# Performance work log

Measured on AMD Instinct MI355X. Metric: run time of the kernel, lower is better.

## Reference

```python
import jax, jax.numpy as jnp
import numpy as np

B, T, E = 64, 64, 256
S, ENC = 128, 1024
RNN, ATT, DENSE = 1024, 1024, 8000


def setup_inputs() -> dict:
    key = jax.random.key(0)
    ks = jax.random.split(key, 16)
    s = 0.02
    return {
        "initial_input": jax.random.normal(ks[0], (B, T, E), jnp.float32),
        "hidden": jax.random.normal(ks[1], (B, RNN), jnp.float32),
        "cell": jax.random.normal(ks[2], (B, RNN), jnp.float32),
        "encoder_output": jax.random.normal(ks[3], (B, S, ENC), jnp.float32),
        "W1": jax.random.normal(ks[4], (RNN, ATT), jnp.float32) * s,
        "b1": jnp.zeros((ATT,), jnp.float32),
        "W2": jax.random.normal(ks[5], (ENC, ATT), jnp.float32) * s,
        "b2": jnp.zeros((ATT,), jnp.float32),
        "V": jax.random.normal(ks[6], (ATT, 1), jnp.float32) * s,
        "bV": jnp.zeros((1,), jnp.float32),
        "kernel": jax.random.normal(ks[7], (ENC + E, 4 * RNN), jnp.float32) * s,
        "rkernel": jax.random.normal(ks[8], (RNN, 4 * RNN), jnp.float32) * s,
        "bias": jnp.zeros((4 * RNN,), jnp.float32),
        "Wd": jax.random.normal(ks[9], (RNN, DENSE), jnp.float32) * s,
        "bd": jnp.zeros((DENSE,), jnp.float32),
        "seq_len": T,
    }


def _decode(initial_input, hidden, cell, encoder_output,
            W1, b1, W2, b2, V, bV, kernel, rkernel, bias, Wd, bd):
    # Keys W2(encoder_output) are step-independent: precompute once. [B,S,ATT]
    keys = jnp.einsum('bse,ea->bsa', encoder_output, W2) + b2

    def step(carry, x_t):
        h, c = carry
        # Bahdanau attention: score = V^T tanh(W1 h + W2 enc)
        q = h @ W1 + b1                                  # [B,ATT]
        score = jnp.tanh(q[:, None, :] + keys) @ V + bV   # [B,S,1]
        attn = jax.nn.softmax(score, axis=1)              # [B,S,1]
        ctx = jnp.sum(attn * encoder_output, axis=1)      # [B,ENC]
        # LSTM cell (Keras gate order i,f,g,o; sigmoid/tanh activations)
        inp = jnp.concatenate([ctx, x_t], axis=-1)        # [B,ENC+E]
        z = inp @ kernel + h @ rkernel + bias              # [B,4*RNN]
        i, f, g, o = jnp.split(z, 4, axis=-1)
        i = jax.nn.sigmoid(i)
        f = jax.nn.sigmoid(f)
        g = jnp.tanh(g)
        o = jax.nn.sigmoid(o)
        c_new = f * c + i * g
        h_new = o * jnp.tanh(c_new)
        logits = h_new @ Wd + bd                           # [B,DENSE]
        return (h_new, c_new), logits

    xs = jnp.swapaxes(initial_input, 0, 1)  # [T,B,E]
    (h, c), logits = jax.lax.scan(step, (hidden, cell), xs)
    outputs = jnp.swapaxes(logits, 0, 1)    # [B,T,DENSE]
    return outputs, h, c


def reference(initial_input, hidden, cell, encoder_output,
              W1, b1, W2, b2, V, bV, kernel, rkernel, bias, Wd, bd, seq_len):
    # seq_len == initial_input.shape[1] (static); the Python loop in the
    # original is expressed as an efficient lax.scan over decode steps.
    return _decode(initial_input[:, :seq_len, :], hidden, cell, encoder_output,
                   W1, b1, W2, b2, V, bV, kernel, rkernel, bias, Wd, bd)
```

## Files before the change

kernel.cpp:

```cpp
#include <hip/hip_runtime.h>
#include <hip/hip_bf16.h>
#include <stdint.h>


typedef __attribute__((ext_vector_type(8))) short short8;
typedef __attribute__((ext_vector_type(4))) float floatx4;
typedef __attribute__((ext_vector_type(4))) unsigned short ushortx4;

__device__ __forceinline__ float b2f(unsigned short u) {
    union { unsigned int i; float f; } v; v.i = ((unsigned int)u) << 16; return v.f;
}
__device__ __forceinline__ unsigned short f2b(float f) {
    union { float f; unsigned int i; } v; v.f = f;
    unsigned int r = v.i + 0x7fffu + ((v.i >> 16) & 1u);
    return (unsigned short)(r >> 16);
}
__device__ __forceinline__ float ftanh(float x) {
    x = fminf(15.f, fmaxf(-15.f, x));
    float e = __expf(2.f * x);
    return (e - 1.f) * __builtin_amdgcn_rcpf(e + 1.f);
}
__device__ __forceinline__ float vtanh(float x) {
    return __builtin_fmaf(-2.f, __builtin_amdgcn_rcpf(__expf(2.f * x) + 1.f), 1.f);
}
__device__ __forceinline__ float fsig(float x) {
    return __builtin_amdgcn_rcpf(1.f + __expf(-x));
}
__device__ __forceinline__ void ld_lds16(const void* g, void* l) {
    __builtin_amdgcn_global_load_lds((const __attribute__((address_space(1))) void*)g,
                                     (__attribute__((address_space(3))) void*)l, 16, 0, 0);
}

__device__ __forceinline__ void tr_tile(
    float (*tile)[33], const float* __restrict__ src, int srcld,
    unsigned short* __restrict__ dst, int dstld, int coloff, int perm,
    int bx, int by, int tid)
{
    const int k0 = by * 32, n0 = bx * 32;
    const int r = tid >> 3, c = (tid & 7) * 4;
    int n = n0 + c;
    int cn = perm ? ((((n >> 4) & 3) << 10) | ((n >> 6) << 4) | (n & 15)) : n;
    float4 v = *(const float4*)&src[(size_t)(k0 + r) * srcld + cn];
    tile[r][c + 0] = v.x; tile[r][c + 1] = v.y;
    tile[r][c + 2] = v.z; tile[r][c + 3] = v.w;
    __syncthreads();
    const int nr = tid >> 3, kc = (tid & 7) * 4;
    ushortx4 o;
    o[0] = f2b(tile[kc + 0][nr]);
    o[1] = f2b(tile[kc + 1][nr]);
    o[2] = f2b(tile[kc + 2][nr]);
    o[3] = f2b(tile[kc + 3][nr]);
    *(ushortx4*)&dst[(size_t)(n0 + nr) * dstld + coloff + k0 + kc] = o;
}

__global__ __launch_bounds__(256) void prep_all(
    const float* __restrict__ W2, unsigned short* __restrict__ W2T,
    const float* __restrict__ W1, unsigned short* __restrict__ W1T,
    const float* __restrict__ Wk, const float* __restrict__ rk,
    unsigned short* __restrict__ KRT,
    const float* __restrict__ Wd, unsigned short* __restrict__ WdT,
    const float* __restrict__ enc, unsigned short* __restrict__ enc_bf,
    const float* __restrict__ hidden, const float* __restrict__ cell,
    const float* __restrict__ x,
    float* __restrict__ cb, unsigned short* __restrict__ hbf,
    unsigned short* __restrict__ Axc0)
{
    __shared__ float tile[32][33];
    const int lid = blockIdx.x, tid = threadIdx.x;
    if (lid < 1024) {
        tr_tile(tile, W2, 1024, W2T, 1024, 0, 0, lid & 31, lid >> 5, tid);
    } else if (lid < 2048) {
        int l = lid - 1024;
        tr_tile(tile, W1, 1024, W1T, 1024, 0, 0, l & 31, l >> 5, tid);
    } else if (lid < 6144) {
        int l = lid - 2048;
        tr_tile(tile, Wk, 4096, KRT, 2304, 0, 1, l & 127, l >> 7, tid);
    } else if (lid < 7168) {
        int l = lid - 6144;
        tr_tile(tile, Wk + 1024 * 4096, 4096, KRT, 2304, 1024, 1, l & 127, l >> 7, tid);
    } else if (lid < 11264) {
        int l = lid - 7168;
        tr_tile(tile, rk, 4096, KRT, 2304, 1280, 1, l & 127, l >> 7, tid);
    } else if (lid < 19264) {
        int l = lid - 11264;
        tr_tile(tile, Wd, 8000, WdT, 1024, 0, 0, l % 250, l / 250, tid);
    } else if (lid < 27456) {
        int i = (lid - 19264) * 256 + tid;
        float4 v = ((const float4*)enc)[i];
        ushortx4 o;
        o[0] = f2b(v.x); o[1] = f2b(v.y); o[2] = f2b(v.z); o[3] = f2b(v.w);
        ((ushortx4*)enc_bf)[i] = o;
    } else if (lid < 27712) {
        int idx = (lid - 27456) * 256 + tid;
        float h = hidden[idx], c = cell[idx];
        cb[idx] = c;
        unsigned short hb = f2b(h);
        hbf[idx] = hb;
        Axc0[(idx >> 10) * 2304 + 1280 + (idx & 1023)] = hb;
    } else {
        int p = (lid - 27712) * 256 + tid;
        int b = p >> 7, e2 = (p & 127) * 2;
        float x0 = x[((size_t)b * 64) * 256 + e2];
        float x1 = x[((size_t)b * 64) * 256 + e2 + 1];
        *(unsigned int*)&Axc0[b * 2304 + 1024 + e2] =
            (unsigned int)f2b(x0) | ((unsigned int)f2b(x1) << 16);
    }
}

__global__ __launch_bounds__(256) void gemm_bf16_128(
    const unsigned short* __restrict__ A, int lda,
    const unsigned short* __restrict__ BT, int ldbt, int K,
    float* __restrict__ Cf, unsigned short* __restrict__ Cb,
    int ldc, int ncols, const float* __restrict__ bias, int swz)
{
    __shared__ __align__(16) unsigned short As[128 * 32];
    __shared__ __align__(16) unsigned short Bs[128 * 32];
    const int tid = threadIdx.x, wave = tid >> 6, lane = tid & 63;
    const int q = lane >> 4, lm = lane & 15;
    const int wr = wave >> 1, wc = wave & 1;
    int bx = blockIdx.x, by = blockIdx.y;
    if (swz == 1) {
        int bid = by * gridDim.x + bx;
        int xcd = bid & 7, l = bid >> 3;
        bx = xcd * 8 + (l & 7);
        by = l >> 3;
    } else if (swz == 2) {
        int bid = by * gridDim.x + bx;
        int xcd = bid & 7, m = bid >> 3;
        by = xcd * 8 + (m & 7);
        bx = m >> 3;
    }
    const int m0 = by * 128, n0 = bx * 128;
    const int srow = lane >> 2;
    const int gch = (lane & 3) ^ ((lane >> 3) & 3);
    const unsigned short* Ag0 = A + (size_t)(m0 + wave * 32 + srow) * lda + gch * 8;
    const unsigned short* Ag1 = Ag0 + (size_t)16 * lda;
    const unsigned short* Bg0 = BT + (size_t)(n0 + wave * 32 + srow) * ldbt + gch * 8;
    const unsigned short* Bg1 = Bg0 + (size_t)16 * ldbt;
    unsigned short* Al0 = &As[(wave * 32) * 32];
    unsigned short* Al1 = &As[(wave * 32 + 16) * 32];
    unsigned short* Bl0 = &Bs[(wave * 32) * 32];
    unsigned short* Bl1 = &Bs[(wave * 32 + 16) * 32];

    const floatx4 z4 = {0.f, 0.f, 0.f, 0.f};
    floatx4 acc[4][4];
#pragma unroll
    for (int i = 0; i < 4; i++)
#pragma unroll
        for (int j = 0; j < 4; j++) acc[i][j] = z4;
    const int ach = ((q ^ ((lm >> 1) & 3))) * 8;

    for (int kb = 0; kb < K; kb += 32) {
        ld_lds16(Ag0 + kb, Al0);
        ld_lds16(Ag1 + kb, Al1);
        ld_lds16(Bg0 + kb, Bl0);
        ld_lds16(Bg1 + kb, Bl1);
        __syncthreads();
        short8 a[4], b[4];
#pragma unroll
        for (int i = 0; i < 4; i++) a[i] = *(const short8*)&As[(wr * 64 + i * 16 + lm) * 32 + ach];
#pragma unroll
        for (int j = 0; j < 4; j++) b[j] = *(const short8*)&Bs[(wc * 64 + j * 16 + lm) * 32 + ach];
#pragma unroll
        for (int i = 0; i < 4; i++)
#pragma unroll
            for (int j = 0; j < 4; j++)
                acc[i][j] = __builtin_amdgcn_mfma_f32_16x16x32_bf16(a[i], b[j], acc[i][j], 0, 0, 0);
        __syncthreads();
    }
    const int rb = m0 + wr * 64 + q * 4;
#pragma unroll
    for (int i = 0; i < 4; i++) {
#pragma unroll
        for (int j = 0; j < 4; j++) {
            int col = n0 + wc * 64 + j * 16 + lm;
            if (col < ncols) {
                float bv = bias ? bias[col] : 0.f;
#pragma unroll
                for (int r = 0; r < 4; r++) {
                    float v = acc[i][j][r] + bv;
                    size_t idx = (size_t)(rb + i * 16 + r) * ldc + col;
                    if (Cf) Cf[idx] = v;
                    if (Cb) Cb[idx] = f2b(v);
                }
            }
        }
    }
}

__global__ __launch_bounds__(256) void gemm64_split(
    const unsigned short* __restrict__ A, int lda,
    const unsigned short* __restrict__ BT, int ldbt,
    int kchunk, float* __restrict__ Cpart, int ldc)
{
    __shared__ __align__(16) unsigned short As[4][64 * 32];
    __shared__ __align__(16) unsigned short Bs[4][64 * 32];
    const int tid = threadIdx.x, wave = tid >> 6, lane = tid & 63;
    const int q = lane >> 4, lm = lane & 15;
    const int n0 = blockIdx.x * 64;
    const int k0 = blockIdx.z * kchunk;
    const int srow = lane >> 2;
    const int gch = (lane & 3) ^ ((lane >> 3) & 3);
    const unsigned short* Ag = A + (size_t)(wave * 16 + srow) * lda + k0 + gch * 8;
    const unsigned short* Bg = BT + (size_t)(n0 + wave * 16 + srow) * ldbt + k0 + gch * 8;
    const int loff = (wave * 16) * 32;
    const floatx4 z4 = {0.f, 0.f, 0.f, 0.f};
    floatx4 acc0 = z4, acc1 = z4, acc2 = z4, acc3 = z4;
    const int ach = ((q ^ ((lm >> 1) & 3))) * 8;
    const int nit = kchunk >> 5;

#pragma unroll
    for (int p = 0; p < 3; ++p) {
        if (p < nit) {
            ld_lds16(Ag + p * 32, &As[p][loff]);
            ld_lds16(Bg + p * 32, &Bs[p][loff]);
        }
    }
    for (int it = 0; it < nit; ++it) {
        const int st = it & 3;
        if (it + 2 < nit)      asm volatile("s_waitcnt vmcnt(4)\n\ts_barrier" ::: "memory");
        else if (it + 1 < nit) asm volatile("s_waitcnt vmcnt(2)\n\ts_barrier" ::: "memory");
        else                   asm volatile("s_waitcnt vmcnt(0)\n\ts_barrier" ::: "memory");
        if (it + 3 < nit) {
            const int sn = (it + 3) & 3;
            ld_lds16(Ag + (it + 3) * 32, &As[sn][loff]);
            ld_lds16(Bg + (it + 3) * 32, &Bs[sn][loff]);
        }
        short8 a  = *(const short8*)&As[st][(wave * 16 + lm) * 32 + ach];
        short8 b0 = *(const short8*)&Bs[st][(0 * 16 + lm) * 32 + ach];
        short8 b1 = *(const short8*)&Bs[st][(1 * 16 + lm) * 32 + ach];
        short8 b2 = *(const short8*)&Bs[st][(2 * 16 + lm) * 32 + ach];
        short8 b3 = *(const short8*)&Bs[st][(3 * 16 + lm) * 32 + ach];
        acc0 = __builtin_amdgcn_mfma_f32_16x16x32_bf16(a, b0, acc0, 0, 0, 0);
        acc1 = __builtin_amdgcn_mfma_f32_16x16x32_bf16(a, b1, acc1, 0, 0, 0);
        acc2 = __builtin_amdgcn_mfma_f32_16x16x32_bf16(a, b2, acc2, 0, 0, 0);
        acc3 = __builtin_amdgcn_mfma_f32_16x16x32_bf16(a, b3, acc3, 0, 0, 0);
    }
    float* Cp = Cpart + (size_t)blockIdx.z * 64 * ldc;
    const int rb = wave * 16 + q * 4;
    floatx4 accs[4] = {acc0, acc1, acc2, acc3};
#pragma unroll
    for (int i = 0; i < 4; i++) {
        int col = n0 + i * 16 + lm;
#pragma unroll
        for (int r = 0; r < 4; r++) Cp[(size_t)(rb + r) * ldc + col] = accs[i][r];
    }
}

__global__ __launch_bounds__(256) void attn_scores(
    const float* __restrict__ qp, const float* __restrict__ b1,
    const unsigned short* __restrict__ keys,
    const float* __restrict__ V, const float* __restrict__ bV,
    float* __restrict__ sc)
{
    __shared__ float qs[1024];
    __shared__ float vs[1024];
    const int b = blockIdx.y, sg = blockIdx.x;
    const int tid = threadIdx.x, wave = tid >> 6, lane = tid & 63;
    {
        float4 a0 = ((const float4*)(qp + (size_t)b * 1024))[tid];
        float4 a1 = ((const float4*)(qp + 65536 + (size_t)b * 1024))[tid];
        float4 a2 = ((const float4*)(qp + 131072 + (size_t)b * 1024))[tid];
        float4 a3 = ((const float4*)(qp + 196608 + (size_t)b * 1024))[tid];
        float4 ab = ((const float4*)b1)[tid];
        float4 av = ((const float4*)V)[tid];
        float4 r;
        r.x = a0.x + a1.x + a2.x + a3.x + ab.x;
        r.y = a0.y + a1.y + a2.y + a3.y + ab.y;
        r.z = a0.z + a1.z + a2.z + a3.z + ab.z;
        r.w = a0.w + a1.w + a2.w + a3.w + ab.w;
        *(float4*)&qs[tid * 4] = r;
        *(float4*)&vs[tid * 4] = av;
    }
    __syncthreads();
    float qr[16], vr[16];
#pragma unroll
    for (int i = 0; i < 4; i++) {
        float4 tq = *(const float4*)&qs[lane * 16 + i * 4];
        float4 tv = *(const float4*)&vs[lane * 16 + i * 4];
        qr[i * 4 + 0] = tq.x; qr[i * 4 + 1] = tq.y; qr[i * 4 + 2] = tq.z; qr[i * 4 + 3] = tq.w;
        vr[i * 4 + 0] = tv.x; vr[i * 4 + 1] = tv.y; vr[i * 4 + 2] = tv.z; vr[i * 4 + 3] = tv.w;
    }
    const float bv0 = bV[0];
#pragma unroll
    for (int i = 0; i < 4; i++) {
        const int s = sg * 16 + wave * 4 + i;
        const uint4* kp = (const uint4*)(keys + ((size_t)(b * 128 + s)) * 1024 + lane * 16);
        uint4 k0 = kp[0], k1 = kp[1];
        float kf[16];
        kf[0] = b2f((unsigned short)(k0.x & 0xffff)); kf[1] = b2f((unsigned short)(k0.x >> 16));
        kf[2] = b2f((unsigned short)(k0.y & 0xffff)); kf[3] = b2f((unsigned short)(k0.y >> 16));
        kf[4] = b2f((unsigned short)(k0.z & 0xffff)); kf[5] = b2f((unsigned short)(k0.z >> 16));
        kf[6] = b2f((unsigned short)(k0.w & 0xffff)); kf[7] = b2f((unsigned short)(k0.w >> 16));
        kf[8] = b2f((unsigned short)(k1.x & 0xffff)); kf[9] = b2f((unsigned short)(k1.x >> 16));
        kf[10] = b2f((unsigned short)(k1.y & 0xffff)); kf[11] = b2f((unsigned short)(k1.y >> 16));
        kf[12] = b2f((unsigned short)(k1.z & 0xffff)); kf[13] = b2f((unsigned short)(k1.z >> 16));
        kf[14] = b2f((unsigned short)(k1.w & 0xffff)); kf[15] = b2f((unsigned short)(k1.w >> 16));
        float part = 0.f;
#pragma unroll
        for (int j = 0; j < 16; j++) part += vr[j] * vtanh(qr[j] + kf[j]);
#pragma unroll
        for (int off = 32; off; off >>= 1) part += __shfl_xor(part, off);
        if (lane == 0) sc[b * 128 + s] = part + bv0;
    }
}

__global__ __launch_bounds__(256) void softmax_ctx(
    const float* __restrict__ sc, const unsigned short* __restrict__ enc_bf,
    unsigned short* __restrict__ Axc_t)
{
    __shared__ float attnv[128];
    __shared__ float red[4][64][2];
    __shared__ float ssum_s;
    const int b = blockIdx.y, chunk = blockIdx.x;
    const int tid = threadIdx.x, wave = tid >> 6, lane = tid & 63;
    if (tid < 128) attnv[tid] = __expf(sc[b * 128 + tid]);
    __syncthreads();
    if (tid < 64) {
        float s2 = attnv[tid] + attnv[tid + 64];
#pragma unroll
        for (int off = 32; off; off >>= 1) s2 += __shfl_xor(s2, off);
        if (tid == 0) ssum_s = s2;
    }
    const unsigned int* ep = (const unsigned int*)enc_bf + (size_t)b * 65536 + chunk * 64 + lane;
    __syncthreads();
    float ax = 0.f, ay = 0.f;
#pragma unroll 8
    for (int i = 0; i < 32; i++) {
        int s = wave * 32 + i;
        float a = attnv[s];
        unsigned int u = ep[(size_t)s * 512];
        ax += a * b2f((unsigned short)(u & 0xffff));
        ay += a * b2f((unsigned short)(u >> 16));
    }
    red[wave][lane][0] = ax; red[wave][lane][1] = ay;
    __syncthreads();
    if (tid < 64) {
        float rs = __builtin_amdgcn_rcpf(ssum_s);
        float fx = (red[0][lane][0] + red[1][lane][0] + red[2][lane][0] + red[3][lane][0]) * rs;
        float fy = (red[0][lane][1] + red[1][lane][1] + red[2][lane][1] + red[3][lane][1]) * rs;
        *(unsigned int*)&Axc_t[b * 2304 + chunk * 128 + lane * 2] =
            (unsigned int)f2b(fx) | ((unsigned int)f2b(fy) << 16);
    }
}

__global__ __launch_bounds__(512) void gemm_gates(
    const unsigned short* __restrict__ Axc_r,
    unsigned short* __restrict__ Axc_w,
    const unsigned short* __restrict__ KRT,
    const float* __restrict__ bz,
    float* __restrict__ cb,
    unsigned short* __restrict__ hbf, unsigned short* __restrict__ Hall,
    const float* __restrict__ x, int t,
    float* __restrict__ out, int last)
{
    __shared__ __align__(16) char smem[65536];
    unsigned short* As = (unsigned short*)smem;
    unsigned short* Bs = (unsigned short*)(smem + 32768);
    float* red = (float*)smem;
    const int tid = threadIdx.x, wave = tid >> 6, lane = tid & 63;
    const int q = lane >> 4, lm = lane & 15;
    const int h = wave >> 2, wm = wave & 3;
    const int bx = blockIdx.x;
    const int srow = lane >> 2;
    const int gch = (lane & 3) ^ ((lane >> 3) & 3);
    const unsigned short* Ag = Axc_r + (size_t)(wm * 16 + srow) * 2304 + h * 1152 + gch * 8;
    const unsigned short* Bg = KRT + (size_t)(bx * 64 + wm * 16 + srow) * 2304 + h * 1152 + gch * 8;
    const int tileoff = h * 2048;
    const int ldoff = tileoff + (wm * 16) * 32;
    const floatx4 z4 = {0.f, 0.f, 0.f, 0.f};
    floatx4 acc0 = z4, acc1 = z4, acc2 = z4, acc3 = z4;
    const int ach = ((q ^ ((lm >> 1) & 3))) * 8;

#pragma unroll
    for (int p = 0; p < 3; ++p) {
        ld_lds16(Ag + p * 32, &As[p * 4096 + ldoff]);
        ld_lds16(Bg + p * 32, &Bs[p * 4096 + ldoff]);
    }
    for (int it = 0; it < 36; ++it) {
        const int st = it & 3;
        if (it < 34)       asm volatile("s_waitcnt vmcnt(4)\n\ts_barrier" ::: "memory");
        else if (it == 34) asm volatile("s_waitcnt vmcnt(2)\n\ts_barrier" ::: "memory");
        else               asm volatile("s_waitcnt vmcnt(0)\n\ts_barrier" ::: "memory");
        if (it + 3 < 36) {
            const int sn = (it + 3) & 3;
            ld_lds16(Ag + (it + 3) * 32, &As[sn * 4096 + ldoff]);
            ld_lds16(Bg + (it + 3) * 32, &Bs[sn * 4096 + ldoff]);
        }
        const unsigned short* Ast = &As[st * 4096 + tileoff];
        const unsigned short* Bst = &Bs[st * 4096 + tileoff];
        short8 a  = *(const short8*)&Ast[(wm * 16 + lm) * 32 + ach];
        short8 b0 = *(const short8*)&Bst[(0 * 16 + lm) * 32 + ach];
        short8 b1 = *(const short8*)&Bst[(1 * 16 + lm) * 32 + ach];
        short8 b2 = *(const short8*)&Bst[(2 * 16 + lm) * 32 + ach];
        short8 b3 = *(const short8*)&Bst[(3 * 16 + lm) * 32 + ach];
        acc0 = __builtin_amdgcn_mfma_f32_16x16x32_bf16(a, b0, acc0, 0, 0, 0);
        acc1 = __builtin_amdgcn_mfma_f32_16x16x32_bf16(a, b1, acc1, 0, 0, 0);
        acc2 = __builtin_amdgcn_mfma_f32_16x16x32_bf16(a, b2, acc2, 0, 0, 0);
        acc3 = __builtin_amdgcn_mfma_f32_16x16x32_bf16(a, b3, acc3, 0, 0, 0);
    }
    __syncthreads();
    if (h == 1) {
        float* rp = &red[(wm * 64 + lane) * 16];
        *(floatx4*)&rp[0]  = acc0; *(floatx4*)&rp[4]  = acc1;
        *(floatx4*)&rp[8]  = acc2; *(floatx4*)&rp[12] = acc3;
        if (t < 63) {
            int local = tid - 256;
            if (local < 128) {
                const float* xp = x + ((size_t)bx * 64 + t + 1) * 256 + local * 2;
                float x0 = xp[0], x1 = xp[1];
                ((unsigned int*)&Axc_w[bx * 2304 + 1024])[local] =
                    (unsigned int)f2b(x0) | ((unsigned int)f2b(x1) << 16);
            }
        }
    }
    __syncthreads();
    if (h == 0) {
        const float* rp = &red[(wm * 64 + lane) * 16];
        acc0 += *(const floatx4*)&rp[0];
        acc1 += *(const floatx4*)&rp[4];
        acc2 += *(const floatx4*)&rp[8];
        acc3 += *(const floatx4*)&rp[12];
        const int col = bx * 16 + lm;
        const float bzi = bz[col], bzf = bz[1024 + col];
        const float bzg = bz[2048 + col], bzo = bz[3072 + col];
#pragma unroll
        for (int r = 0; r < 4; ++r) {
            const int b = wm * 16 + q * 4 + r;
            float zi = acc0[r] + bzi;
            float zf = acc1[r] + bzf;
            float zg = acc2[r] + bzg;
            float zo = acc3[r] + bzo;
            float ii = fsig(zi), ff = fsig(zf), gg = ftanh(zg), oo = fsig(zo);
            const int idx = b * 1024 + col;
            float cn = ff * cb[idx] + ii * gg;
            float hn = oo * ftanh(cn);
            cb[idx] = cn;
            unsigned short hb = f2b(hn);
            hbf[idx] = hb;
            Hall[((size_t)b * 64 + t) * 1024 + col] = hb;
            if (t < 63) Axc_w[b * 2304 + 1280 + col] = hb;
            if (last) {
                out[32768000 + idx] = hn;
                out[32768000 + 65536 + idx] = cn;
            }
        }
    }
}

extern "C" void kernel_launch(void* const* d_in, const int* in_sizes, int n_in,
                              void* d_out, int out_size, void* d_ws, size_t ws_size,
                              hipStream_t stream)
{
    const float* x      = (const float*)d_in[0];
    const float* hidden = (const float*)d_in[1];
    const float* cell   = (const float*)d_in[2];
    const float* enc    = (const float*)d_in[3];
    const float* W1     = (const float*)d_in[4];
    const float* b1     = (const float*)d_in[5];
    const float* W2     = (const float*)d_in[6];
    const float* b2     = (const float*)d_in[7];
    const float* V      = (const float*)d_in[8];
    const float* bV     = (const float*)d_in[9];
    const float* Wk     = (const float*)d_in[10];
    const float* rk     = (const float*)d_in[11];
    const float* bz     = (const float*)d_in[12];
    const float* Wd     = (const float*)d_in[13];
    const float* bd     = (const float*)d_in[14];
    float* out = (float*)d_out;

    char* ws = (char*)d_ws;
    unsigned short* enc_bf  = (unsigned short*)(ws + 0);
    unsigned short* keys_bf = (unsigned short*)(ws + 16777216);
    unsigned short* W1T     = (unsigned short*)(ws + 33554432);
    unsigned short* KRT     = (unsigned short*)(ws + 35651584);
    unsigned short* WdT     = (unsigned short*)(ws + 54525952);
    unsigned short* Hall    = (unsigned short*)(ws + 71303168);
    unsigned short* W2T     = Hall;
    unsigned short* Axc     = (unsigned short*)(ws + 79691776);
    float* qp    = (float*)(ws + 80281600);
    unsigned short* hbf     = (unsigned short*)(ws + 81330176);
    float* scbuf = (float*)(ws + 81461248);
    float* cb    = (float*)(ws + 81494016);

    prep_all<<<27744, 256, 0, stream>>>(W2, W2T, W1, W1T, Wk, rk, KRT, Wd, WdT,
                                        enc, enc_bf, hidden, cell, x, cb, hbf, Axc);

    gemm_bf16_128<<<dim3(8, 64), 256, 0, stream>>>(enc_bf, 1024, W2T, 1024, 1024,
                                                   nullptr, keys_bf, 1024, 1024, b2, 2);

    for (int t = 0; t < 64; t++) {
        unsigned short* Axc_r = Axc + (size_t)(t & 1) * 147456;
        unsigned short* Axc_w = Axc + (size_t)((t + 1) & 1) * 147456;
        gemm64_split<<<dim3(16, 1, 4), 256, 0, stream>>>(hbf, 1024, W1T, 1024, 256, qp, 1024);
        attn_scores<<<dim3(8, 64), 256, 0, stream>>>(qp, b1, keys_bf, V, bV, scbuf);
        softmax_ctx<<<dim3(8, 64), 256, 0, stream>>>(scbuf, enc_bf, Axc_r);
        gemm_gates<<<64, 512, 0, stream>>>(Axc_r, Axc_w, KRT, bz, cb, hbf, Hall,
                                           x, t, out, (t == 63) ? 1 : 0);
    }

    gemm_bf16_128<<<dim3(64, 32), 256, 0, stream>>>(Hall, 1024, WdT, 1024, 1024,
                                                    out, nullptr, 8000, 8000, bd, 1);
}
```

Baseline: 2.315 ms.

## Multi-stage LDS pipeline in bf16 GEMM and wider split-K for query projection

The 128x128 bf16 GEMM now uses a 4-buffer LDS ring with three tiles of async global-to-LDS loads in flight. Each iteration waits with an explicit vmcnt and a single barrier instead of a load-then-sync loop with two barriers. Separately, the per-step query projection splits K eight ways instead of four, and attn_scores sums eight partials, with workspace offsets moved to fit the larger partial buffer. The aim is to hide load latency in the big keys and dense GEMMs and to put more blocks on the small per-step GEMM. The cost is four times the LDS per block, which may reduce occupancy, plus extra partial-sum traffic.

```diff
diff --git a/kernel.cpp b/kernel.cpp
--- a/kernel.cpp
+++ b/kernel.cpp
@@ -113,8 +113,8 @@
     float* __restrict__ Cf, unsigned short* __restrict__ Cb,
     int ldc, int ncols, const float* __restrict__ bias, int swz)
 {
-    __shared__ __align__(16) unsigned short As[128 * 32];
-    __shared__ __align__(16) unsigned short Bs[128 * 32];
+    __shared__ __align__(16) unsigned short As[4][128 * 32];
+    __shared__ __align__(16) unsigned short Bs[4][128 * 32];
     const int tid = threadIdx.x, wave = tid >> 6, lane = tid & 63;
     const int q = lane >> 4, lm = lane & 15;
     const int wr = wave >> 1, wc = wave & 1;
@@ -137,10 +137,8 @@
     const unsigned short* Ag1 = Ag0 + (size_t)16 * lda;
     const unsigned short* Bg0 = BT + (size_t)(n0 + wave * 32 + srow) * ldbt + gch * 8;
     const unsigned short* Bg1 = Bg0 + (size_t)16 * ldbt;
-    unsigned short* Al0 = &As[(wave * 32) * 32];
-    unsigned short* Al1 = &As[(wave * 32 + 16) * 32];
-    unsigned short* Bl0 = &Bs[(wave * 32) * 32];
-    unsigned short* Bl1 = &Bs[(wave * 32 + 16) * 32];
+    const int l0 = (wave * 32) * 32;
+    const int l1 = (wave * 32 + 16) * 32;
 
     const floatx4 z4 = {0.f, 0.f, 0.f, 0.f};
     floatx4 acc[4][4];
@@ -149,24 +147,39 @@
 #pragma unroll
         for (int j = 0; j < 4; j++) acc[i][j] = z4;
     const int ach = ((q ^ ((lm >> 1) & 3))) * 8;
-
-    for (int kb = 0; kb < K; kb += 32) {
-        ld_lds16(Ag0 + kb, Al0);
-        ld_lds16(Ag1 + kb, Al1);
-        ld_lds16(Bg0 + kb, Bl0);
-        ld_lds16(Bg1 + kb, Bl1);
-        __syncthreads();
+    const int nit = K >> 5;
+
+#pragma unroll
+    for (int p = 0; p < 3; ++p) {
+        if (p < nit) {
+            ld_lds16(Ag0 + p * 32, &As[p][l0]);
+            ld_lds16(Ag1 + p * 32, &As[p][l1]);
+            ld_lds16(Bg0 + p * 32, &Bs[p][l0]);
+            ld_lds16(Bg1 + p * 32, &Bs[p][l1]);
+        }
+    }
+    for (int it = 0; it < nit; ++it) {
+        const int st = it & 3;
+        if (it + 2 < nit)      asm volatile("s_waitcnt vmcnt(8)\n\ts_barrier" ::: "memory");
+        else if (it + 1 < nit) asm volatile("s_waitcnt vmcnt(4)\n\ts_barrier" ::: "memory");
+        else                   asm volatile("s_waitcnt vmcnt(0)\n\ts_barrier" ::: "memory");
+        if (it + 3 < nit) {
+            const int sn = (it + 3) & 3;
+            ld_lds16(Ag0 + (it + 3) * 32, &As[sn][l0]);
+            ld_lds16(Ag1 + (it + 3) * 32, &As[sn][l1]);
+            ld_lds16(Bg0 + (it + 3) * 32, &Bs[sn][l0]);
+            ld_lds16(Bg1 + (it + 3) * 32, &Bs[sn][l1]);
+        }
         short8 a[4], b[4];
 #pragma unroll
-        for (int i = 0; i < 4; i++) a[i] = *(const short8*)&As[(wr * 64 + i * 16 + lm) * 32 + ach];
-#pragma unroll
-        for (int j = 0; j < 4; j++) b[j] = *(const short8*)&Bs[(wc * 64 + j * 16 + lm) * 32 + ach];
+        for (int i = 0; i < 4; i++) a[i] = *(const short8*)&As[st][(wr * 64 + i * 16 + lm) * 32 + ach];
+#pragma unroll
+        for (int j = 0; j < 4; j++) b[j] = *(const short8*)&Bs[st][(wc * 64 + j * 16 + lm) * 32 + ach];
 #pragma unroll
         for (int i = 0; i < 4; i++)
 #pragma unroll
             for (int j = 0; j < 4; j++)
                 acc[i][j] = __builtin_amdgcn_mfma_f32_16x16x32_bf16(a[i], b[j], acc[i][j], 0, 0, 0);
-        __syncthreads();
     }
     const int rb = m0 + wr * 64 + q * 4;
 #pragma unroll
@@ -258,19 +271,14 @@
     const int b = blockIdx.y, sg = blockIdx.x;
     const int tid = threadIdx.x, wave = tid >> 6, lane = tid & 63;
     {
-        float4 a0 = ((const float4*)(qp + (size_t)b * 1024))[tid];
-        float4 a1 = ((const float4*)(qp + 65536 + (size_t)b * 1024))[tid];
-        float4 a2 = ((const float4*)(qp + 131072 + (size_t)b * 1024))[tid];
-        float4 a3 = ((const float4*)(qp + 196608 + (size_t)b * 1024))[tid];
-        float4 ab = ((const float4*)b1)[tid];
-        float4 av = ((const float4*)V)[tid];
-        float4 r;
-        r.x = a0.x + a1.x + a2.x + a3.x + ab.x;
-        r.y = a0.y + a1.y + a2.y + a3.y + ab.y;
-        r.z = a0.z + a1.z + a2.z + a3.z + ab.z;
-        r.w = a0.w + a1.w + a2.w + a3.w + ab.w;
+        float4 r = ((const float4*)b1)[tid];
+#pragma unroll
+        for (int p = 0; p < 8; ++p) {
+            float4 a = ((const float4*)(qp + (size_t)p * 65536 + (size_t)b * 1024))[tid];
+            r.x += a.x; r.y += a.y; r.z += a.z; r.w += a.w;
+        }
         *(float4*)&qs[tid * 4] = r;
-        *(float4*)&vs[tid * 4] = av;
+        *(float4*)&vs[tid * 4] = ((const float4*)V)[tid];
     }
     __syncthreads();
     float qr[16], vr[16];
@@ -479,9 +487,9 @@
     unsigned short* W2T     = Hall;
     unsigned short* Axc     = (unsigned short*)(ws + 79691776);
     float* qp    = (float*)(ws + 80281600);
-    unsigned short* hbf     = (unsigned short*)(ws + 81330176);
-    float* scbuf = (float*)(ws + 81461248);
-    float* cb    = (float*)(ws + 81494016);
+    unsigned short* hbf     = (unsigned short*)(ws + 82378752);
+    float* scbuf = (float*)(ws + 82509824);
+    float* cb    = (float*)(ws + 82542592);
 
     prep_all<<<27744, 256, 0, stream>>>(W2, W2T, W1, W1T, Wk, rk, KRT, Wd, WdT,
                                         enc, enc_bf, hidden, cell, x, cb, hbf, Axc);
@@ -492,7 +500,7 @@
     for (int t = 0; t < 64; t++) {
         unsigned short* Axc_r = Axc + (size_t)(t & 1) * 147456;
         unsigned short* Axc_w = Axc + (size_t)((t + 1) & 1) * 147456;
-        gemm64_split<<<dim3(16, 1, 4), 256, 0, stream>>>(hbf, 1024, W1T, 1024, 256, qp, 1024);
+        gemm64_split<<<dim3(16, 1, 8), 256, 0, stream>>>(hbf, 1024, W1T, 1024, 128, qp, 1024);
         attn_scores<<<dim3(8, 64), 256, 0, stream>>>(qp, b1, keys_bf, V, bV, scbuf);
         softmax_ctx<<<dim3(8, 64), 256, 0, stream>>>(scbuf, enc_bf, Axc_r);
         gemm_gates<<<64, 512, 0, stream>>>(Axc_r, Axc_w, KRT, bz, cb, hbf, Hall,
```

Result: no change. 2.326 ms (+0.4%).
